# Kernel tuning notes

Measured on AMD Instinct MI355X. Metric: run time of the kernel, lower is better.

The kernel has to match this reference:

```python
import jax, jax.numpy as jnp
import numpy as np

B, N, C = 8, 2048, 256
H = 8
D = C // H
HID = 4 * C
EPS = 1e-5


def _layernorm(x, g, b):
    m = jnp.mean(x, axis=-1, keepdims=True)
    v = jnp.mean((x - m) ** 2, axis=-1, keepdims=True)
    return (x - m) * jax.lax.rsqrt(v + EPS) * g + b


def setup_inputs() -> dict:
    key = jax.random.key(0)
    ks = jax.random.split(key, 8)
    s = 0.02
    return {
        "x": jax.random.normal(ks[0], (B, N, C), dtype=jnp.float32),
        "ln1_g": jnp.ones((C,), jnp.float32),
        "ln1_b": jnp.zeros((C,), jnp.float32),
        "qkv_w": jax.random.normal(ks[1], (3 * C, C), jnp.float32) * s,  # torch Linear: (out,in), no bias
        "scale": jnp.asarray(D ** -0.5, jnp.float32),  # learnable temperature scalar
        "proj_w": jax.random.normal(ks[2], (C, C), jnp.float32) * s,
        "proj_b": jnp.zeros((C,), jnp.float32),
        "ln2_g": jnp.ones((C,), jnp.float32),
        "ln2_b": jnp.zeros((C,), jnp.float32),
        "fc1_w": jax.random.normal(ks[3], (HID, C), jnp.float32) * s,
        "fc1_b": jnp.zeros((HID,), jnp.float32),
        "fc2_w": jax.random.normal(ks[4], (C, HID), jnp.float32) * s,
        "fc2_b": jnp.zeros((C,), jnp.float32),
    }


def _attn(x, qkv_w, scale, proj_w, proj_b):
    b, n, c = x.shape
    qkv = (x @ qkv_w.T).reshape(b, n, 3, H, D)
    qkv = jnp.transpose(qkv, (2, 0, 3, 1, 4))  # (3, B, H, N, D)
    q, k, v = qkv[0], qkv[1], qkv[2]
    attn = jnp.einsum("bhnd,bhmd->bhnm", q, k) * scale  # full NxN scores (faithful)
    eye = jnp.eye(n, dtype=bool)
    attn = jnp.where(eye, -jnp.inf, attn)  # mask diagonal (no self-relation)
    attn = jax.nn.softmax(attn, axis=-1)
    out = jnp.einsum("bhnm,bhmd->bhnd", attn, v)
    out = jnp.transpose(out, (0, 2, 1, 3)).reshape(b, n, c)
    return out @ proj_w.T + proj_b


def reference(x, ln1_g, ln1_b, qkv_w, scale, proj_w, proj_b,
              ln2_g, ln2_b, fc1_w, fc1_b, fc2_w, fc2_b):
    x = x + _attn(_layernorm(x, ln1_g, ln1_b), qkv_w, scale, proj_w, proj_b)
    h = _layernorm(x, ln2_g, ln2_b)
    h = jax.nn.gelu(h @ fc1_w.T + fc1_b, approximate=False)  # torch GELU default = exact
    x = x + (h @ fc2_w.T + fc2_b)
    return x
```

## Files before the change

### kernel.cpp

```cpp
#include <hip/hip_runtime.h>
#include <cstdint>
#include <cstddef>


typedef __bf16 bf16x8 __attribute__((ext_vector_type(8)));
typedef __bf16 bf16x4 __attribute__((ext_vector_type(4)));
typedef float  f32x4  __attribute__((ext_vector_type(4)));

#define BN_TOK   2048
#define CC       256
#define HID_DIM  1024
#define MROWS    16384

#define OFF_W    0u
#define OFF_A    1572864u
#define OFF_QKV  9961472u
#define OFF_H    35127296u
#define WOFF_QKV 0
#define WOFF_PRJ 196608
#define WOFF_FC1 262144
#define WOFF_FC2 524288

__device__ __forceinline__ void gload_lds16(const __bf16* g, __bf16* l) {
    __builtin_amdgcn_global_load_lds(
        (const __attribute__((address_space(1))) void*)g,
        (__attribute__((address_space(3))) void*)l, 16, 0, 0);
}

__global__ __launch_bounds__(256) void cvt_w_kernel(
    const float* __restrict__ q, const float* __restrict__ p,
    const float* __restrict__ f1, const float* __restrict__ f2,
    __bf16* __restrict__ dst)
{
    int i = (blockIdx.x * 256 + threadIdx.x) * 4;
    const float* src; int off;
    if (i < 196608)      { src = q;  off = 0; }
    else if (i < 262144) { src = p;  off = 196608; }
    else if (i < 524288) { src = f1; off = 262144; }
    else                 { src = f2; off = 524288; }
    float4 v = *(const float4*)(src + (i - off));
    bf16x4 o;
    o[0] = (__bf16)v.x; o[1] = (__bf16)v.y; o[2] = (__bf16)v.z; o[3] = (__bf16)v.w;
    *(bf16x4*)(dst + i) = o;
}

__global__ __launch_bounds__(256) void ln_kernel(
    const float* __restrict__ x, const float* __restrict__ g,
    const float* __restrict__ b, __bf16* __restrict__ y)
{
    const int lane = threadIdx.x & 63;
    const int row  = blockIdx.x * 4 + (threadIdx.x >> 6);
    const float4 xv = *(const float4*)(x + (size_t)row * CC + lane * 4);
    float s  = xv.x + xv.y + xv.z + xv.w;
    float s2 = xv.x*xv.x + xv.y*xv.y + xv.z*xv.z + xv.w*xv.w;
#pragma unroll
    for (int m = 1; m < 64; m <<= 1) {
        s  += __shfl_xor(s,  m);
        s2 += __shfl_xor(s2, m);
    }
    const float mean = s * (1.0f / 256.0f);
    const float var  = fmaxf(s2 * (1.0f / 256.0f) - mean * mean, 0.0f);
    const float rstd = rsqrtf(var + 1e-5f);
    const float4 gv = *(const float4*)(g + lane * 4);
    const float4 bv = *(const float4*)(b + lane * 4);
    bf16x4 o;
    o[0] = (__bf16)((xv.x - mean) * rstd * gv.x + bv.x);
    o[1] = (__bf16)((xv.y - mean) * rstd * gv.y + bv.y);
    o[2] = (__bf16)((xv.z - mean) * rstd * gv.z + bv.z);
    o[3] = (__bf16)((xv.w - mean) * rstd * gv.w + bv.w);
    *(bf16x4*)(y + (size_t)row * CC + lane * 4) = o;
}

__global__ __launch_bounds__(256) void ln_bf_kernel(
    const __bf16* __restrict__ x, const float* __restrict__ g,
    const float* __restrict__ b, __bf16* __restrict__ y)
{
    const int lane = threadIdx.x & 63;
    const int row  = blockIdx.x * 4 + (threadIdx.x >> 6);
    const bf16x4 xv = *(const bf16x4*)&x[(size_t)row * CC + lane * 4];
    float x0 = (float)xv[0], x1 = (float)xv[1], x2 = (float)xv[2], x3 = (float)xv[3];
    float s  = x0 + x1 + x2 + x3;
    float s2 = x0*x0 + x1*x1 + x2*x2 + x3*x3;
#pragma unroll
    for (int m = 1; m < 64; m <<= 1) {
        s  += __shfl_xor(s,  m);
        s2 += __shfl_xor(s2, m);
    }
    const float mean = s * (1.0f / 256.0f);
    const float var  = fmaxf(s2 * (1.0f / 256.0f) - mean * mean, 0.0f);
    const float rstd = rsqrtf(var + 1e-5f);
    const float4 gv = *(const float4*)(g + lane * 4);
    const float4 bv = *(const float4*)(b + lane * 4);
    bf16x4 o;
    o[0] = (__bf16)((x0 - mean) * rstd * gv.x + bv.x);
    o[1] = (__bf16)((x1 - mean) * rstd * gv.y + bv.y);
    o[2] = (__bf16)((x2 - mean) * rstd * gv.z + bv.z);
    o[3] = (__bf16)((x3 - mean) * rstd * gv.w + bv.w);
    *(bf16x4*)(y + (size_t)row * CC + lane * 4) = o;
}

template<int BM, int BIAS, int GELU, int RES, int RESBF, int OUTBF, int VSPLIT>
__global__ __launch_bounds__(256) void gemm_k(
    const __bf16* __restrict__ A, const __bf16* __restrict__ W,
    const float* __restrict__ bias, const void* __restrict__ resv,
    void* __restrict__ outp, __bf16* __restrict__ vT, int M, int N, int K)
{
    constexpr int MI  = BM / 32;
    constexpr int ASZ = BM * 32;
    __shared__ __align__(16) __bf16 As[3 * ASZ];
    __shared__ __align__(16) __bf16 Bs[3 * 4096];
    const int tid = threadIdx.x, lane = tid & 63, wid = tid >> 6;
    const int wr = wid >> 1, wc = wid & 1;
    const int fr = lane & 15, fg = lane >> 4;
    const int tm = blockIdx.x * BM, tn = blockIdx.y * 128;

    const int lrow = lane >> 2, lk = (lane & 3) * 8;
    const __bf16* gA = A + (size_t)(tm + (BM == 128 ? wid * 32 : wid * 16) + lrow) * K + lk;
    const __bf16* gB = W + (size_t)(tn + wid * 32 + lrow) * K + lk;
    const size_t rowK16 = (size_t)16 * K;
    const int aoff = (BM == 128 ? wid * 1024 : wid * 512);
    const int boff = wid * 1024;

    const int KT = K >> 5;

    auto STAGE = [&](int kt, int buf) {
        const int k0 = kt * 32;
        __bf16* lA = As + buf * ASZ + aoff;
        __bf16* lB = Bs + buf * 4096 + boff;
        gload_lds16(gA + k0, lA);
        if (BM == 128) gload_lds16(gA + rowK16 + k0, lA + 512);
        gload_lds16(gB + k0, lB);
        gload_lds16(gB + rowK16 + k0, lB + 512);
    };

    f32x4 acc[MI][4];
    const f32x4 vz = {0.f, 0.f, 0.f, 0.f};
#pragma unroll
    for (int mi = 0; mi < MI; ++mi)
#pragma unroll
        for (int nj = 0; nj < 4; ++nj) acc[mi][nj] = vz;

    STAGE(0, 0);
    STAGE(1 < KT ? 1 : 0, 1);
    if (BM == 128) asm volatile("s_waitcnt vmcnt(4)" ::: "memory");
    else           asm volatile("s_waitcnt vmcnt(3)" ::: "memory");
    __builtin_amdgcn_s_barrier();

    int cur = 0;
    for (int k = 0; k < KT; ++k) {
        int nt = k + 2; if (nt > KT - 1) nt = KT - 1;
        int sb = cur + 2; if (sb >= 3) sb -= 3;
        STAGE(nt, sb);

        const __bf16* bA = As + cur * ASZ;
        const __bf16* bB = Bs + cur * 4096;
        bf16x8 af[MI], bfv[4];
#pragma unroll
        for (int mi = 0; mi < MI; ++mi)
            af[mi] = *(const bf16x8*)&bA[(wr * (BM / 2) + mi * 16 + fr) * 32 + fg * 8];
#pragma unroll
        for (int nj = 0; nj < 4; ++nj)
            bfv[nj] = *(const bf16x8*)&bB[(wc * 64 + nj * 16 + fr) * 32 + fg * 8];
#pragma unroll
        for (int mi = 0; mi < MI; ++mi)
#pragma unroll
            for (int nj = 0; nj < 4; ++nj)
                acc[mi][nj] = __builtin_amdgcn_mfma_f32_16x16x32_bf16(
                    af[mi], bfv[nj], acc[mi][nj], 0, 0, 0);

        if (BM == 128) asm volatile("s_waitcnt vmcnt(4)" ::: "memory");
        else           asm volatile("s_waitcnt vmcnt(3)" ::: "memory");
        __builtin_amdgcn_s_barrier();
        cur += 1; if (cur == 3) cur = 0;
    }
    asm volatile("s_waitcnt vmcnt(0)" ::: "memory");

    if (VSPLIT && tn >= 512) {
#pragma unroll
        for (int mi = 0; mi < MI; ++mi) {
#pragma unroll
            for (int nj = 0; nj < 4; ++nj) {
                const int dfull = tn - 512 + wc * 64 + nj * 16 + fr;
                const int row0  = tm + wr * (BM / 2) + mi * 16 + fg * 4;
                const int bb = row0 >> 11;
                const int n0 = row0 & 2047;
                bf16x4 pk;
                pk[0] = (__bf16)acc[mi][nj][0]; pk[1] = (__bf16)acc[mi][nj][1];
                pk[2] = (__bf16)acc[mi][nj][2]; pk[3] = (__bf16)acc[mi][nj][3];
                *(bf16x4*)&vT[((size_t)(bb * 8 + (dfull >> 5)) * 32 + (dfull & 31)) * 2048 + n0] = pk;
            }
        }
        return;
    }

#pragma unroll
    for (int mi = 0; mi < MI; ++mi) {
#pragma unroll
        for (int nj = 0; nj < 4; ++nj) {
            const int col = tn + wc * 64 + nj * 16 + fr;
            float bv = 0.0f;
            if (BIAS) bv = bias[col];
#pragma unroll
            for (int r = 0; r < 4; ++r) {
                const int row = tm + wr * (BM / 2) + mi * 16 + fg * 4 + r;
                float v = acc[mi][nj][r];
                if (BIAS) v += bv;
                if (GELU) v = v * 0.5f * (1.0f + erff(v * 0.70710678118654752f));
                if (RES) {
                    if (RESBF) v += (float)((const __bf16*)resv)[(size_t)row * N + col];
                    else       v += ((const float*)resv)[(size_t)row * N + col];
                }
                if (OUTBF) ((__bf16*)outp)[(size_t)row * N + col] = (__bf16)v;
                else       ((float*)outp)[(size_t)row * N + col]  = v;
            }
        }
    }
}

__global__ __launch_bounds__(256) void attn_kernel(
    const __bf16* __restrict__ qkv, const __bf16* __restrict__ vT,
    const float* __restrict__ scale_p, __bf16* __restrict__ ao)
{
    __shared__ __align__(16) __bf16 Ks[3 * 2048];
    __shared__ __align__(16) __bf16 Vs[3 * 2048];
    __shared__ __align__(16) unsigned char PsT[4][4096];

    const int tid = threadIdx.x, lane = tid & 63, wid = tid >> 6;
    const int fr = lane & 15, fg = lane >> 4;
    const int qt = blockIdx.x;
    const int bh = blockIdx.y;
    const int b = bh >> 3, h = bh & 7;
    const float c = scale_p[0] * 1.4426950408889634f;
    const size_t base = (size_t)b * BN_TOK * 768;
    const int hq = h * 32, hk = 256 + h * 32;
    const int ib = qt * 128 + wid * 32;

    const bf16x8 q0 = *(const bf16x8*)&qkv[base + (size_t)(ib + fr) * 768 + hq + fg * 8];
    const bf16x8 q1 = *(const bf16x8*)&qkv[base + (size_t)(ib + 16 + fr) * 768 + hq + fg * 8];
    bf16x8 qf[2];
#pragma unroll
    for (int e = 0; e < 8; ++e) {
        qf[0][e] = (__bf16)((float)q0[e] * c);
        qf[1][e] = (__bf16)((float)q1[e] * c);
    }
    bf16x8 onesb;
#pragma unroll
    for (int e = 0; e < 8; ++e) onesb[e] = (__bf16)1.0f;

    const f32x4 vz = {0.f, 0.f, 0.f, 0.f};
    f32x4 accd[2][2];
    accd[0][0] = vz; accd[0][1] = vz; accd[1][0] = vz; accd[1][1] = vz;
    f32x4 accp[2]; accp[0] = vz; accp[1] = vz;

    const int srow = tid >> 2;
    const int kblk = ((tid & 3) ^ (srow & 3)) * 8;
    const __bf16* ksrc = qkv + base + (size_t)srow * 768 + hk + kblk;
    const int vd   = tid >> 3;
    const int vblk = ((tid & 7) ^ (vd & 7)) * 8;
    const __bf16* vsrc = vT + ((size_t)(bh * 32 + vd)) * 2048 + vblk;
    __bf16* kdw = Ks + wid * 512;
    __bf16* vdw = Vs + wid * 512;

    auto STAGE = [&](int nt, int buf) {
        gload_lds16(ksrc + (size_t)nt * 64 * 768, kdw + buf * 2048);
        gload_lds16(vsrc + nt * 64,               vdw + buf * 2048);
    };

    unsigned char* pst = &PsT[wid][0];
    const int swz = (fr & 7) << 4;

    STAGE(0, 0);
    STAGE(1, 1);
    asm volatile("s_waitcnt vmcnt(2)" ::: "memory");
    __builtin_amdgcn_s_barrier();

    int cur = 0;
    for (int jt = 0; jt < 32; ++jt) {
        const int jb = jt * 64;
        int nt = jt + 2; if (nt > 31) nt = 31;
        int sb = cur + 2; if (sb >= 3) sb -= 3;
        STAGE(nt, sb);

        const __bf16* kb = Ks + cur * 2048;
        const __bf16* vbuf = Vs + cur * 2048;
        bf16x8 kf[4], vb[2][2];
#pragma unroll
        for (int nj = 0; nj < 4; ++nj)
            kf[nj] = *(const bf16x8*)&kb[(nj * 16 + fr) * 32 + ((fg ^ (fr & 3)) * 8)];
#pragma unroll
        for (int ka = 0; ka < 2; ++ka)
#pragma unroll
            for (int dh = 0; dh < 2; ++dh)
                vb[ka][dh] = *(const bf16x8*)&vbuf[(dh * 16 + fr) * 64 + (((ka * 4 + fg) ^ (fr & 7)) * 8)];

        const bool dmask = (jb < ib + 32) && (ib < jb + 64);

#pragma unroll
        for (int mi = 0; mi < 2; ++mi) {
            f32x4 s[4];
#pragma unroll
            for (int nj = 0; nj < 4; ++nj)
                s[nj] = __builtin_amdgcn_mfma_f32_16x16x32_bf16(kf[nj], qf[mi], vz, 0, 0, 0);
#pragma unroll
            for (int nj = 0; nj < 4; ++nj)
#pragma unroll
                for (int r = 0; r < 4; ++r)
                    s[nj][r] = exp2f(s[nj][r]);
            if (dmask) {
                const int gi = ib + mi * 16 + fr;
#pragma unroll
                for (int nj = 0; nj < 4; ++nj) {
                    const int gj = jb + nj * 16 + fg * 4;
#pragma unroll
                    for (int r = 0; r < 4; ++r)
                        if (gj + r == gi) s[nj][r] = 0.f;
                }
            }
            unsigned char* pr = pst + (mi * 16 + fr) * 128;
#pragma unroll
            for (int nj = 0; nj < 4; ++nj) {
                bf16x4 pk;
                pk[0] = (__bf16)s[nj][0]; pk[1] = (__bf16)s[nj][1];
                pk[2] = (__bf16)s[nj][2]; pk[3] = (__bf16)s[nj][3];
                *(bf16x4*)(pr + ((nj * 32 + fg * 8) ^ swz)) = pk;
            }
        }
#pragma unroll
        for (int mi = 0; mi < 2; ++mi) {
            unsigned char* pr = pst + (mi * 16 + fr) * 128;
#pragma unroll
            for (int ka = 0; ka < 2; ++ka) {
                const bf16x8 pa = *(const bf16x8*)(pr + ((ka * 64 + fg * 16) ^ swz));
#pragma unroll
                for (int dh = 0; dh < 2; ++dh)
                    accd[mi][dh] = __builtin_amdgcn_mfma_f32_16x16x32_bf16(
                        pa, vb[ka][dh], accd[mi][dh], 0, 0, 0);
                accp[mi] = __builtin_amdgcn_mfma_f32_16x16x32_bf16(
                    pa, onesb, accp[mi], 0, 0, 0);
            }
        }
        asm volatile("s_waitcnt vmcnt(2)" ::: "memory");
        __builtin_amdgcn_s_barrier();
        cur += 1; if (cur == 3) cur = 0;
    }
    asm volatile("s_waitcnt vmcnt(0)" ::: "memory");

#pragma unroll
    for (int mi = 0; mi < 2; ++mi)
#pragma unroll
        for (int dh = 0; dh < 2; ++dh)
#pragma unroll
            for (int r = 0; r < 4; ++r) {
                const int i = ib + mi * 16 + fg * 4 + r;
                const float o = accd[mi][dh][r] / accp[mi][r];
                ao[(size_t)(b * BN_TOK + i) * CC + h * 32 + dh * 16 + fr] = (__bf16)o;
            }
}

extern "C" void kernel_launch(void* const* d_in, const int* in_sizes, int n_in,
                              void* d_out, int out_size, void* d_ws, size_t ws_size,
                              hipStream_t stream)
{
    const float* x      = (const float*)d_in[0];
    const float* ln1_g  = (const float*)d_in[1];
    const float* ln1_b  = (const float*)d_in[2];
    const float* qkv_w  = (const float*)d_in[3];
    const float* scale  = (const float*)d_in[4];
    const float* proj_w = (const float*)d_in[5];
    const float* proj_b = (const float*)d_in[6];
    const float* ln2_g  = (const float*)d_in[7];
    const float* ln2_b  = (const float*)d_in[8];
    const float* fc1_w  = (const float*)d_in[9];
    const float* fc1_b  = (const float*)d_in[10];
    const float* fc2_w  = (const float*)d_in[11];
    const float* fc2_b  = (const float*)d_in[12];

    char* ws = (char*)d_ws;
    __bf16* wbf   = (__bf16*)(ws + OFF_W);
    __bf16* abf   = (__bf16*)(ws + OFF_A);
    __bf16* qkvbf = (__bf16*)(ws + OFF_QKV);
    __bf16* x1bf  = (__bf16*)(ws + OFF_QKV);
    __bf16* vT    = (__bf16*)(ws + OFF_H);
    __bf16* hbf   = (__bf16*)(ws + OFF_H);
    float*  out   = (float*)d_out;

    cvt_w_kernel<<<768, 256, 0, stream>>>(qkv_w, proj_w, fc1_w, fc2_w, wbf);
    ln_kernel<<<4096, 256, 0, stream>>>(x, ln1_g, ln1_b, abf);
    gemm_k<128,0,0,0,0,1,1><<<dim3(128,6), 256, 0, stream>>>(
        abf, wbf + WOFF_QKV, nullptr, nullptr, qkvbf, vT, MROWS, 768, 256);
    attn_kernel<<<dim3(16,64), 256, 0, stream>>>(qkvbf, vT, scale, abf);
    gemm_k<64,1,0,1,0,1,0><<<dim3(256,2), 256, 0, stream>>>(
        abf, wbf + WOFF_PRJ, proj_b, x, x1bf, nullptr, MROWS, 256, 256);
    ln_bf_kernel<<<4096, 256, 0, stream>>>(x1bf, ln2_g, ln2_b, abf);
    gemm_k<128,1,1,0,0,1,0><<<dim3(128,8), 256, 0, stream>>>(
        abf, wbf + WOFF_FC1, fc1_b, nullptr, hbf, nullptr, MROWS, HID_DIM, 256);
    gemm_k<64,1,0,1,1,0,0><<<dim3(256,2), 256, 0, stream>>>(
        hbf, wbf + WOFF_FC2, fc2_b, x1bf, out, nullptr, MROWS, 256, HID_DIM);
}
```

Baseline: 261.8 us.

## Use 32x32x16 MFMA in attention with in-register P transpose via permlane32 swap

Rewrites the attention inner loop to use 32x32x16 bf16 MFMAs instead of 16x16x32. The exponentiated score tile now stays in registers and is rearranged into the A-operand layout with v_permlane32_swap, so the per-wave LDS staging buffer for P is removed. It also replaces exp2f with a raw v_exp_f32 and simplifies the diagonal mask test. This removes LDS write/read traffic and fewer, larger MFMA issues, but it depends on the 32x32 accumulator layout mapping being exactly right.

```diff
diff --git a/kernel.cpp b/kernel.cpp
--- a/kernel.cpp
+++ b/kernel.cpp
@@ -6,6 +6,7 @@
 typedef __bf16 bf16x8 __attribute__((ext_vector_type(8)));
 typedef __bf16 bf16x4 __attribute__((ext_vector_type(4)));
 typedef float  f32x4  __attribute__((ext_vector_type(4)));
+typedef float  f32x16 __attribute__((ext_vector_type(16)));
 
 #define BN_TOK   2048
 #define CC       256
@@ -25,6 +26,18 @@
     __builtin_amdgcn_global_load_lds(
         (const __attribute__((address_space(1))) void*)g,
         (__attribute__((address_space(3))) void*)l, 16, 0, 0);
+}
+
+__device__ __forceinline__ float fexp2(float x) {
+    float r;
+    asm("v_exp_f32 %0, %1" : "=v"(r) : "v"(x));
+    return r;
+}
+
+__device__ __forceinline__ unsigned pk2(float lo, float hi) {
+    union { __bf16 b[2]; unsigned u; } t;
+    t.b[0] = (__bf16)lo; t.b[1] = (__bf16)hi;
+    return t.u;
 }
 
 __global__ __launch_bounds__(256) void cvt_w_kernel(
@@ -223,39 +236,38 @@
 {
     __shared__ __align__(16) __bf16 Ks[3 * 2048];
     __shared__ __align__(16) __bf16 Vs[3 * 2048];
-    __shared__ __align__(16) unsigned char PsT[4][4096];
 
     const int tid = threadIdx.x, lane = tid & 63, wid = tid >> 6;
-    const int fr = lane & 15, fg = lane >> 4;
-    const int qt = blockIdx.x;
-    const int bh = blockIdx.y;
+    const int l31 = lane & 31, hi = lane >> 5;
+    const int qt = blockIdx.x, bh = blockIdx.y;
     const int b = bh >> 3, h = bh & 7;
     const float c = scale_p[0] * 1.4426950408889634f;
     const size_t base = (size_t)b * BN_TOK * 768;
     const int hq = h * 32, hk = 256 + h * 32;
     const int ib = qt * 128 + wid * 32;
 
-    const bf16x8 q0 = *(const bf16x8*)&qkv[base + (size_t)(ib + fr) * 768 + hq + fg * 8];
-    const bf16x8 q1 = *(const bf16x8*)&qkv[base + (size_t)(ib + 16 + fr) * 768 + hq + fg * 8];
+    const __bf16* qrow = qkv + base + (size_t)(ib + l31) * 768 + hq;
     bf16x8 qf[2];
-#pragma unroll
-    for (int e = 0; e < 8; ++e) {
-        qf[0][e] = (__bf16)((float)q0[e] * c);
-        qf[1][e] = (__bf16)((float)q1[e] * c);
+    {
+        const bf16x8 t0 = *(const bf16x8*)(qrow + hi * 8);
+        const bf16x8 t1 = *(const bf16x8*)(qrow + 16 + hi * 8);
+#pragma unroll
+        for (int e = 0; e < 8; ++e) {
+            qf[0][e] = (__bf16)((float)t0[e] * c);
+            qf[1][e] = (__bf16)((float)t1[e] * c);
+        }
     }
     bf16x8 onesb;
 #pragma unroll
     for (int e = 0; e < 8; ++e) onesb[e] = (__bf16)1.0f;
 
-    const f32x4 vz = {0.f, 0.f, 0.f, 0.f};
-    f32x4 accd[2][2];
-    accd[0][0] = vz; accd[0][1] = vz; accd[1][0] = vz; accd[1][1] = vz;
-    f32x4 accp[2]; accp[0] = vz; accp[1] = vz;
+    f32x16 accd = {};
+    f32x16 accp = {};
 
     const int srow = tid >> 2;
     const int kblk = ((tid & 3) ^ (srow & 3)) * 8;
     const __bf16* ksrc = qkv + base + (size_t)srow * 768 + hk + kblk;
-    const int vd   = tid >> 3;
+    const int vd = tid >> 3;
     const int vblk = ((tid & 7) ^ (vd & 7)) * 8;
     const __bf16* vsrc = vT + ((size_t)(bh * 32 + vd)) * 2048 + vblk;
     __bf16* kdw = Ks + wid * 512;
@@ -265,9 +277,6 @@
         gload_lds16(ksrc + (size_t)nt * 64 * 768, kdw + buf * 2048);
         gload_lds16(vsrc + nt * 64,               vdw + buf * 2048);
     };
-
-    unsigned char* pst = &PsT[wid][0];
-    const int swz = (fr & 7) << 4;
 
     STAGE(0, 0);
     STAGE(1, 1);
@@ -281,80 +290,62 @@
         int sb = cur + 2; if (sb >= 3) sb -= 3;
         STAGE(nt, sb);
 
-        const __bf16* kb = Ks + cur * 2048;
-        const __bf16* vbuf = Vs + cur * 2048;
-        bf16x8 kf[4], vb[2][2];
-#pragma unroll
-        for (int nj = 0; nj < 4; ++nj)
-            kf[nj] = *(const bf16x8*)&kb[(nj * 16 + fr) * 32 + ((fg ^ (fr & 3)) * 8)];
-#pragma unroll
-        for (int ka = 0; ka < 2; ++ka)
-#pragma unroll
-            for (int dh = 0; dh < 2; ++dh)
-                vb[ka][dh] = *(const bf16x8*)&vbuf[(dh * 16 + fr) * 64 + (((ka * 4 + fg) ^ (fr & 7)) * 8)];
-
-        const bool dmask = (jb < ib + 32) && (ib < jb + 64);
-
-#pragma unroll
-        for (int mi = 0; mi < 2; ++mi) {
-            f32x4 s[4];
-#pragma unroll
-            for (int nj = 0; nj < 4; ++nj)
-                s[nj] = __builtin_amdgcn_mfma_f32_16x16x32_bf16(kf[nj], qf[mi], vz, 0, 0, 0);
-#pragma unroll
-            for (int nj = 0; nj < 4; ++nj)
-#pragma unroll
-                for (int r = 0; r < 4; ++r)
-                    s[nj][r] = exp2f(s[nj][r]);
-            if (dmask) {
-                const int gi = ib + mi * 16 + fr;
-#pragma unroll
-                for (int nj = 0; nj < 4; ++nj) {
-                    const int gj = jb + nj * 16 + fg * 4;
-#pragma unroll
-                    for (int r = 0; r < 4; ++r)
-                        if (gj + r == gi) s[nj][r] = 0.f;
-                }
+        const char* kb   = (const char*)(Ks + cur * 2048);
+        const char* vbuf = (const char*)(Vs + cur * 2048);
+
+        bf16x8 vb[2][2];
+#pragma unroll
+        for (int sub = 0; sub < 2; ++sub)
+#pragma unroll
+            for (int ka = 0; ka < 2; ++ka)
+                vb[sub][ka] = *(const bf16x8*)(vbuf + l31 * 128 +
+                                (((sub * 4 + ka * 2 + hi) ^ (l31 & 7)) << 4));
+
+#pragma unroll
+        for (int sub = 0; sub < 2; ++sub) {
+            const int jrow = sub * 32 + l31;
+            const bf16x8 kf0 = *(const bf16x8*)(kb + jrow * 64 + (((hi)     ^ (jrow & 3)) << 4));
+            const bf16x8 kf1 = *(const bf16x8*)(kb + jrow * 64 + (((2 + hi) ^ (jrow & 3)) << 4));
+            f32x16 s = {};
+            s = __builtin_amdgcn_mfma_f32_32x32x16_bf16(kf0, qf[0], s, 0, 0, 0);
+            s = __builtin_amdgcn_mfma_f32_32x32x16_bf16(kf1, qf[1], s, 0, 0, 0);
+#pragma unroll
+            for (int r = 0; r < 16; ++r) s[r] = fexp2(s[r]);
+            if (jb + sub * 32 == ib) {
+#pragma unroll
+                for (int r = 0; r < 16; ++r)
+                    if (((r & 3) + 8 * (r >> 2) + 4 * hi) == l31) s[r] = 0.f;
             }
-            unsigned char* pr = pst + (mi * 16 + fr) * 128;
-#pragma unroll
-            for (int nj = 0; nj < 4; ++nj) {
-                bf16x4 pk;
-                pk[0] = (__bf16)s[nj][0]; pk[1] = (__bf16)s[nj][1];
-                pk[2] = (__bf16)s[nj][2]; pk[3] = (__bf16)s[nj][3];
-                *(bf16x4*)(pr + ((nj * 32 + fg * 8) ^ swz)) = pk;
-            }
-        }
-#pragma unroll
-        for (int mi = 0; mi < 2; ++mi) {
-            unsigned char* pr = pst + (mi * 16 + fr) * 128;
+            unsigned dw[4][2];
+#pragma unroll
+            for (int q = 0; q < 4; ++q)
+#pragma unroll
+                for (int hh = 0; hh < 2; ++hh)
+                    dw[q][hh] = pk2(s[4 * q + 2 * hh], s[4 * q + 2 * hh + 1]);
 #pragma unroll
             for (int ka = 0; ka < 2; ++ka) {
-                const bf16x8 pa = *(const bf16x8*)(pr + ((ka * 64 + fg * 16) ^ swz));
-#pragma unroll
-                for (int dh = 0; dh < 2; ++dh)
-                    accd[mi][dh] = __builtin_amdgcn_mfma_f32_16x16x32_bf16(
-                        pa, vb[ka][dh], accd[mi][dh], 0, 0, 0);
-                accp[mi] = __builtin_amdgcn_mfma_f32_16x16x32_bf16(
-                    pa, onesb, accp[mi], 0, 0, 0);
+                asm("v_permlane32_swap_b32 %0, %1"
+                    : "+v"(dw[2 * ka][0]), "+v"(dw[2 * ka + 1][0]));
+                asm("v_permlane32_swap_b32 %0, %1"
+                    : "+v"(dw[2 * ka][1]), "+v"(dw[2 * ka + 1][1]));
+                union { unsigned u[4]; bf16x8 v; } pt;
+                pt.u[0] = dw[2 * ka][0];     pt.u[1] = dw[2 * ka][1];
+                pt.u[2] = dw[2 * ka + 1][0]; pt.u[3] = dw[2 * ka + 1][1];
+                accd = __builtin_amdgcn_mfma_f32_32x32x16_bf16(pt.v, vb[sub][ka], accd, 0, 0, 0);
+                accp = __builtin_amdgcn_mfma_f32_32x32x16_bf16(pt.v, onesb,      accp, 0, 0, 0);
             }
         }
         asm volatile("s_waitcnt vmcnt(2)" ::: "memory");
         __builtin_amdgcn_s_barrier();
         cur += 1; if (cur == 3) cur = 0;
     }
-    asm volatile("s_waitcnt vmcnt(0)" ::: "memory");
-
-#pragma unroll
-    for (int mi = 0; mi < 2; ++mi)
-#pragma unroll
-        for (int dh = 0; dh < 2; ++dh)
-#pragma unroll
-            for (int r = 0; r < 4; ++r) {
-                const int i = ib + mi * 16 + fg * 4 + r;
-                const float o = accd[mi][dh][r] / accp[mi][r];
-                ao[(size_t)(b * BN_TOK + i) * CC + h * 32 + dh * 16 + fr] = (__bf16)o;
-            }
+
+#pragma unroll
+    for (int r = 0; r < 16; ++r) {
+        const int i = ib + (r & 3) + 8 * (r >> 2) + 4 * hi;
+        const float o = accd[r] / accp[r];
+        ao[(size_t)(b * BN_TOK + i) * CC + h * 32 + l31] = (__bf16)o;
+    }
 }
 
 extern "C" void kernel_launch(void* const* d_in, const int* in_sizes, int n_in,
```

After: 247.9 us. 5.3% less time.
